# Performance work log

Hardware: AMD Instinct MI355X
Metric: run time of the kernel (lower is better)

Reference implementation:

```python
import jax, jax.numpy as jnp
import numpy as np

N_X = 3
NE = 2048
Emin = 1.0
Emax = 100.0


def setup_inputs() -> dict:
    key = jax.random.key(0)
    k1, k2, k3, k4 = jax.random.split(key, 4)
    # log-spaced energy grid (MeV); code assumes E_grid[0] == Emin
    E_grid = jnp.logspace(np.log10(Emin), np.log10(Emax), NE, dtype=jnp.float32)
    # rates O(1), kernels small -> diagonally dominant per-step system, stable recursion
    R = 1.0 + jax.random.uniform(k1, (N_X, NE), dtype=jnp.float32)
    K = 1e-3 * jax.random.uniform(k2, (N_X, N_X, NE, NE), dtype=jnp.float32)
    S0 = jax.random.uniform(k3, (N_X,), dtype=jnp.float32)
    SC = jax.random.uniform(k4, (N_X, NE), dtype=jnp.float32)
    T = jnp.float32(0.01)
    return {"E_grid": E_grid, "R": R, "K": K, "S0": S0, "SC": SC, "T": T}


def _solve_cascade(E_grid, R, K, S0, SC, T):
    n_x, ne = R.shape
    dy = jnp.log(E_grid[-1] / Emin) / (ne - 1)

    src_last = S0 / R[:, -1]  # (N_X,) : S0[Xp] / R[Xp, -1]
    # boundary value at highest energy: FX_E0[X] = SC[X,-1]/R[X,-1] + sum_Xp K[X,Xp,-1,-1]*S0[Xp]/(R[Xp,-1]*R[X,-1])
    FX_E0 = SC[:, -1] / R[:, -1] + (K[:, :, -1, -1] @ src_last) / R[:, -1]
    F0 = jnp.zeros((n_x, ne), dtype=E_grid.dtype).at[:, -1].set(FX_E0)

    jidx = jnp.arange(ne)

    def step(F, i):
        Ki = K[:, :, i, :]  # (N_X, N_X, NE) slice at outer grid point i
        # trapezoid weights over j: dy*E[j] for i < j < NE-1, half-weight at j = NE-1, 0 elsewhere
        w = jnp.where((jidx > i) & (jidx < ne - 1), dy * E_grid, jnp.zeros((), E_grid.dtype))
        w = w.at[-1].set(0.5 * dy * E_grid[-1])
        # a[X] = SC[X,i] + sum_Xp,j Ki[X,Xp,j] * w[j] * F[Xp,j] + sum_Xp Ki[X,Xp,-1]*S0[Xp]/R[Xp,-1]
        a = SC[:, i] + jnp.einsum('xpj,pj->x', Ki, w * F) + Ki[:, :, -1] @ src_last
        # B[X,Xp] = -0.5*dy*E[i]*K[X,Xp,i,i] + R[X,i]*delta(X,Xp)
        B = -0.5 * dy * E_grid[i] * Ki[:, :, i] + jnp.diag(R[:, i])
        F = F.at[:, i].set(jnp.linalg.solve(B, a))
        return F, None

    idx = jnp.arange(ne - 2, -1, -1)  # backward sweep i = NE-2 ... 0
    F_grid, _ = jax.lax.scan(step, F0, idx)

    approx_zero = jnp.asarray(1e-200, F_grid.dtype)  # underflows to 0 in fp32, matching clamp intent
    F_grid = jnp.where(F_grid > approx_zero, F_grid, approx_zero)

    # sol: row 0 = E_grid, rows 1..N_X = spectra
    return jnp.concatenate([E_grid[None, :], F_grid], axis=0)


def reference(E_grid, R, K, S0, SC, T):
    return _solve_cascade(E_grid, R, K, S0, SC, T)
```

## Files before the change

### kernel.cpp

```cpp
#include <hip/hip_runtime.h>
#include <cstddef>
#include <cstdint>

#define NE 2048
#define NX 3
#define NROWS (NE - 1)
#define BS 64
#define BR (3 * BS)
#define NBLK 32
#define NPAIR 16
#define NCH 8
#define CHS 8
#define CHQ (CHS * 9 * BS)
#define TTH 512
#define PERTH (CHQ / TTH)


static __device__ __forceinline__ float dy_of(const float* E) {
    return logf(E[NE - 1] / E[0]) / (float)(NE - 1);
}

#define DOT4(a, b) ((a).x * (b).x + (a).y * (b).y + (a).z * (b).z + (a).w * (b).w)
#define FMA4(acc, s, b) { (acc).x += (s) * (b).x; (acc).y += (s) * (b).y; \
                          (acc).z += (s) * (b).z; (acc).w += (s) * (b).w; }

__global__ void k_init(const float* __restrict__ E, const float* __restrict__ R,
                       const float* __restrict__ K, const float* __restrict__ S0,
                       const float* __restrict__ SC,
                       float* __restrict__ out, float* __restrict__ wf,
                       float* __restrict__ acc) {
    int i = blockIdx.x * blockDim.x + threadIdx.x;
    if (i >= NE) return;
    const size_t PL = (size_t)NE * NE;
    float dy = dy_of(E);
    float wlast = 0.5f * dy * E[NE - 1];
    float srcl[NX], Fl[NX];
#pragma unroll
    for (int p = 0; p < NX; ++p) srcl[p] = S0[p] / R[p * NE + NE - 1];
#pragma unroll
    for (int x = 0; x < NX; ++x) {
        float s = SC[x * NE + NE - 1];
#pragma unroll
        for (int p = 0; p < NX; ++p)
            s += K[(size_t)(x * NX + p) * PL + (size_t)(NE - 1) * NE + (NE - 1)] * srcl[p];
        Fl[x] = s / R[x * NE + NE - 1];
    }
    out[i] = E[i];
    if (i == NE - 1) {
#pragma unroll
        for (int x = 0; x < NX; ++x) {
            out[(1 + x) * NE + i] = Fl[x] > 0.f ? Fl[x] : 0.f;
            wf[x * NE + i] = wlast * Fl[x];
            acc[x * NE + i] = 0.f;
        }
        return;
    }
#pragma unroll
    for (int x = 0; x < NX; ++x) {
        float s = SC[x * NE + i];
#pragma unroll
        for (int p = 0; p < NX; ++p)
            s += K[(size_t)(x * NX + p) * PL + (size_t)i * NE + (NE - 1)] *
                 (wlast * Fl[p] + srcl[p]);
        acc[x * NE + i] = s;
    }
}

__global__ __launch_bounds__(TTH) void k_tinv(const float* __restrict__ E,
                                              const float* __restrict__ R,
                                              const float* __restrict__ K,
                                              float* __restrict__ G) {
    __shared__ float4 Xs4[BS][BS + 1];
    __shared__ float Kst[CHS][BS][12];
    __shared__ float Binv[BS][9];
    __shared__ float wloc[BS];
    const size_t PL = (size_t)NE * NE;
    int b = blockIdx.x;
    int g = blockIdx.y;
    int i0 = b * BS;
    int tid = threadIdx.x;
    float dy = dy_of(E);

    if (tid < BS) {
        int j = i0 + tid;
        wloc[tid] = (j < NE - 1) ? dy * E[j] : 0.f;
        int ii = tid, i = i0 + ii;
        float b00, b01, b02, b10, b11, b12, b20, b21, b22;
        if (i < NROWS) {
            float h = -0.5f * dy * E[i];
            size_t d = (size_t)i * NE + i;
            b00 = h * K[0 * PL + d] + R[0 * NE + i];
            b01 = h * K[1 * PL + d];
            b02 = h * K[2 * PL + d];
            b10 = h * K[3 * PL + d];
            b11 = h * K[4 * PL + d] + R[1 * NE + i];
            b12 = h * K[5 * PL + d];
            b20 = h * K[6 * PL + d];
            b21 = h * K[7 * PL + d];
            b22 = h * K[8 * PL + d] + R[2 * NE + i];
        } else {
            b00 = 1.f; b01 = 0.f; b02 = 0.f;
            b10 = 0.f; b11 = 1.f; b12 = 0.f;
            b20 = 0.f; b21 = 0.f; b22 = 1.f;
        }
        float C00 = b11 * b22 - b12 * b21;
        float C01 = -(b10 * b22 - b12 * b20);
        float C02 = b10 * b21 - b11 * b20;
        float C10 = -(b01 * b22 - b02 * b21);
        float C11 = b00 * b22 - b02 * b20;
        float C12 = -(b00 * b21 - b01 * b20);
        float C20 = b01 * b12 - b02 * b11;
        float C21 = -(b00 * b12 - b02 * b10);
        float C22 = b00 * b11 - b01 * b10;
        float inv = 1.f / (b00 * C00 + b01 * C01 + b02 * C02);
        Binv[ii][0] = C00 * inv; Binv[ii][1] = C10 * inv; Binv[ii][2] = C20 * inv;
        Binv[ii][3] = C01 * inv; Binv[ii][4] = C11 * inv; Binv[ii][5] = C21 * inv;
        Binv[ii][6] = C02 * inv; Binv[ii][7] = C12 * inv; Binv[ii][8] = C22 * inv;
    }
    __syncthreads();

    float rg[PERTH];
#pragma unroll
    for (int k = 0; k < PERTH; ++k) {
        int q = tid + k * TTH;
        int s = q / (9 * BS);
        int pair = (q / BS) % 9;
        int jj = q & (BS - 1);
        int row = i0 + (BS - 1) - s;
        rg[k] = K[(size_t)pair * PL + (size_t)row * NE + (i0 + jj)];
    }

    int cloc = tid >> 3, sub = tid & 7;
    int colb = g * BS + cloc;

    for (int c = 0; c < NCH; ++c) {
        if (c > 0) __syncthreads();
#pragma unroll
        for (int k = 0; k < PERTH; ++k) {
            int q = tid + k * TTH;
            int s = q / (9 * BS);
            int pair = (q / BS) % 9;
            int jj = q & (BS - 1);
            Kst[s][jj][4 * (pair / 3) + (pair % 3)] = rg[k] * wloc[jj];
        }
        __syncthreads();
        if (c + 1 < NCH) {
#pragma unroll
            for (int k = 0; k < PERTH; ++k) {
                int q = tid + k * TTH;
                int s = q / (9 * BS);
                int pair = (q / BS) % 9;
                int jj = q & (BS - 1);
                int row = i0 + (BS - 1) - ((c + 1) * CHS + s);
                rg[k] = K[(size_t)pair * PL + (size_t)row * NE + (i0 + jj)];
            }
        }
        for (int s = 0; s < CHS; ++s) {
            int ii = (BS - 1) - (c * CHS + s);
            int i = i0 + ii;
            float v0 = 0.f, v1 = 0.f, v2 = 0.f;
            if (sub == 0) {
                v0 = (colb == 3 * ii + 0) ? 1.f : 0.f;
                v1 = (colb == 3 * ii + 1) ? 1.f : 0.f;
                v2 = (colb == 3 * ii + 2) ? 1.f : 0.f;
            }
            if (i < NROWS) {
                for (int jj = ii + 1 + sub; jj < BS; jj += 8) {
                    const float* kp = &Kst[s][jj][0];
                    float4 k0 = *(const float4*)(kp);
                    float4 k1 = *(const float4*)(kp + 4);
                    float4 k2 = *(const float4*)(kp + 8);
                    float4 xv = Xs4[jj][cloc];
                    v0 += k0.x * xv.x + k0.y * xv.y + k0.z * xv.z;
                    v1 += k1.x * xv.x + k1.y * xv.y + k1.z * xv.z;
                    v2 += k2.x * xv.x + k2.y * xv.y + k2.z * xv.z;
                }
            }
            v0 += __shfl_xor(v0, 1); v0 += __shfl_xor(v0, 2); v0 += __shfl_xor(v0, 4);
            v1 += __shfl_xor(v1, 1); v1 += __shfl_xor(v1, 2); v1 += __shfl_xor(v1, 4);
            v2 += __shfl_xor(v2, 1); v2 += __shfl_xor(v2, 2); v2 += __shfl_xor(v2, 4);
            if (sub == 0) {
                float f0, f1, f2;
                if (i < NROWS) {
                    const float* bv = Binv[ii];
                    f0 = bv[0] * v0 + bv[1] * v1 + bv[2] * v2;
                    f1 = bv[3] * v0 + bv[4] * v1 + bv[5] * v2;
                    f2 = bv[6] * v0 + bv[7] * v1 + bv[8] * v2;
                } else {
                    f0 = v0; f1 = v1; f2 = v2;
                }
                Xs4[ii][cloc] = make_float4(f0, f1, f2, 0.f);
            }
            __builtin_amdgcn_wave_barrier();
        }
    }
    __syncthreads();
    float* Gb = G + (size_t)b * BR * BR;
    for (int t = tid; t < BS * BR; t += TTH) {
        int cl = t % BS;
        int rp = t / BS;
        int x = rp >> 6, ii = rp & 63;
        int cb = g * BS + cl;
        int jjc = cb / 3, pc = cb % 3;
        Gb[(size_t)rp * BR + (pc * 64 + jjc)] = ((const float*)&Xs4[ii][cl])[x];
    }
}

__global__ __launch_bounds__(256) void k_gops1(const float* __restrict__ K,
                                               const float* __restrict__ G,
                                               float* __restrict__ ops1) {
    int s = blockIdx.x, ty_ = blockIdx.y, tz = blockIdx.z;
    int rt = tz / 3, ct = tz % 3;
    int t = ty_ + 1;
    float* O = ops1 + (size_t)(s * 3 + ty_) * BR * BR;
    int tid = threadIdx.x;
    if (s + t > NBLK - 1) {
        for (int q = tid; q < 64 * 64; q += 256)
            O[(size_t)(rt * 64 + q / 64) * BR + ct * 64 + (q % 64)] = 0.f;
        return;
    }
    const size_t PL = (size_t)NE * NE;
    const float* Ga = G + (size_t)s * BR * BR;
    int tgt0 = (s + t) * 64;
    int tx = tid & 15, ty = tid >> 4;
    int row0 = rt * 64 + ty * 4;
    int c0 = tx * 4;
    bool maskLast = (s + t == NBLK - 1) && (tx == 15);
    float4 acc0 = {0, 0, 0, 0}, acc1 = {0, 0, 0, 0};
    float4 acc2 = {0, 0, 0, 0}, acc3 = {0, 0, 0, 0};
    for (int k0 = 0; k0 < BR; k0 += 4) {
        int x = k0 >> 6;
        const float* Bb = K + (size_t)(x * 3 + ct) * PL +
                          (size_t)(s * 64 + (k0 & 63)) * NE + tgt0 + c0;
        float4 b0 = *(const float4*)(Bb);
        float4 b1 = *(const float4*)(Bb + NE);
        float4 b2 = *(const float4*)(Bb + 2 * NE);
        float4 b3 = *(const float4*)(Bb + 3 * NE);
        if (maskLast) { b0.w = 0.f; b1.w = 0.f; b2.w = 0.f; b3.w = 0.f; }
        float4 a0 = *(const float4*)(Ga + (size_t)(row0 + 0) * BR + k0);
        float4 a1 = *(const float4*)(Ga + (size_t)(row0 + 1) * BR + k0);
        float4 a2 = *(const float4*)(Ga + (size_t)(row0 + 2) * BR + k0);
        float4 a3 = *(const float4*)(Ga + (size_t)(row0 + 3) * BR + k0);
        FMA4(acc0, a0.x, b0); FMA4(acc0, a0.y, b1); FMA4(acc0, a0.z, b2); FMA4(acc0, a0.w, b3);
        FMA4(acc1, a1.x, b0); FMA4(acc1, a1.y, b1); FMA4(acc1, a1.z, b2); FMA4(acc1, a1.w, b3);
        FMA4(acc2, a2.x, b0); FMA4(acc2, a2.y, b1); FMA4(acc2, a2.z, b2); FMA4(acc2, a2.w, b3);
        FMA4(acc3, a3.x, b0); FMA4(acc3, a3.y, b1); FMA4(acc3, a3.z, b2); FMA4(acc3, a3.w, b3);
    }
    float* Ob = O + (size_t)row0 * BR + ct * 64 + c0;
    *(float4*)(Ob + 0 * BR) = acc0;
    *(float4*)(Ob + 1 * BR) = acc1;
    *(float4*)(Ob + 2 * BR) = acc2;
    *(float4*)(Ob + 3 * BR) = acc3;
}

__global__ __launch_bounds__(256) void k_gops2(const float* __restrict__ E,
                                               const float* __restrict__ G,
                                               const float* __restrict__ ops1,
                                               float* __restrict__ pr) {
    int m = blockIdx.x, w = blockIdx.y, tz = blockIdx.z;
    int rt = tz / 3, ct = tz % 3;
    int A = 2 * m, C = 2 * m + 1;
    int tid = threadIdx.x;
    float dy = dy_of(E);
    const float* Asrc = ops1 + (size_t)(A * 3 + 0) * BR * BR;
    const float* Bsrc = (w == 0) ? (G + (size_t)C * BR * BR)
                                 : (ops1 + (size_t)(C * 3 + (w - 1)) * BR * BR);
    const float* Dsrc = (w == 0) ? nullptr : (ops1 + (size_t)(A * 3 + w) * BR * BR);
    float* O = pr + (size_t)(m * 3 + w) * BR * BR;
    int tx = tid & 15, ty = tid >> 4;
    int row0 = rt * 64 + ty * 4;
    int c0 = ct * 64 + tx * 4;
    float4 acc0 = {0, 0, 0, 0}, acc1 = {0, 0, 0, 0};
    float4 acc2 = {0, 0, 0, 0}, acc3 = {0, 0, 0, 0};
    for (int k0 = 0; k0 < BR; k0 += 4) {
        int e0 = C * 64 + (k0 & 63);
        float w0 = (e0 + 0 < NROWS) ? dy * E[e0 + 0] : 0.f;
        float w1 = (e0 + 1 < NROWS) ? dy * E[e0 + 1] : 0.f;
        float w2 = (e0 + 2 < NROWS) ? dy * E[e0 + 2] : 0.f;
        float w3 = (e0 + 3 < NROWS) ? dy * E[e0 + 3] : 0.f;
        const float* Bb = Bsrc + (size_t)k0 * BR + c0;
        float4 b0 = *(const float4*)(Bb + 0 * BR);
        float4 b1 = *(const float4*)(Bb + 1 * BR);
        float4 b2 = *(const float4*)(Bb + 2 * BR);
        float4 b3 = *(const float4*)(Bb + 3 * BR);
        b0.x *= w0; b0.y *= w0; b0.z *= w0; b0.w *= w0;
        b1.x *= w1; b1.y *= w1; b1.z *= w1; b1.w *= w1;
        b2.x *= w2; b2.y *= w2; b2.z *= w2; b2.w *= w2;
        b3.x *= w3; b3.y *= w3; b3.z *= w3; b3.w *= w3;
        float4 a0 = *(const float4*)(Asrc + (size_t)(row0 + 0) * BR + k0);
        float4 a1 = *(const float4*)(Asrc + (size_t)(row0 + 1) * BR + k0);
        float4 a2 = *(const float4*)(Asrc + (size_t)(row0 + 2) * BR + k0);
        float4 a3 = *(const float4*)(Asrc + (size_t)(row0 + 3) * BR + k0);
        FMA4(acc0, a0.x, b0); FMA4(acc0, a0.y, b1); FMA4(acc0, a0.z, b2); FMA4(acc0, a0.w, b3);
        FMA4(acc1, a1.x, b0); FMA4(acc1, a1.y, b1); FMA4(acc1, a1.z, b2); FMA4(acc1, a1.w, b3);
        FMA4(acc2, a2.x, b0); FMA4(acc2, a2.y, b1); FMA4(acc2, a2.z, b2); FMA4(acc2, a2.w, b3);
        FMA4(acc3, a3.x, b0); FMA4(acc3, a3.y, b1); FMA4(acc3, a3.z, b2); FMA4(acc3, a3.w, b3);
    }
    float* Ob = O + (size_t)row0 * BR + c0;
    if (Dsrc) {
        const float* Db = Dsrc + (size_t)row0 * BR + c0;
        float4 d0 = *(const float4*)(Db + 0 * BR);
        float4 d1 = *(const float4*)(Db + 1 * BR);
        float4 d2 = *(const float4*)(Db + 2 * BR);
        float4 d3 = *(const float4*)(Db + 3 * BR);
        acc0.x += d0.x; acc0.y += d0.y; acc0.z += d0.z; acc0.w += d0.w;
        acc1.x += d1.x; acc1.y += d1.y; acc1.z += d1.z; acc1.w += d1.w;
        acc2.x += d2.x; acc2.y += d2.y; acc2.z += d2.z; acc2.w += d2.w;
        acc3.x += d3.x; acc3.y += d3.y; acc3.z += d3.z; acc3.w += d3.w;
    }
    *(float4*)(Ob + 0 * BR) = acc0;
    *(float4*)(Ob + 1 * BR) = acc1;
    *(float4*)(Ob + 2 * BR) = acc2;
    *(float4*)(Ob + 3 * BR) = acc3;
}

__global__ __launch_bounds__(512) void k_pair2(const float* __restrict__ E,
                                               const float* __restrict__ K,
                                               const float* __restrict__ G,
                                               const float* __restrict__ ops1,
                                               const float* __restrict__ pr,
                                               float* __restrict__ acc,
                                               float* __restrict__ wf,
                                               float* __restrict__ out,
                                               int m, int hasV) {
    const size_t PL = (size_t)NE * NE;
    int A = 2 * m, C = 2 * m + 1;
    int tid = threadIdx.x;
    int bid = blockIdx.x;
    int lane = tid & 63, wv = tid >> 6;

    if (bid >= 12) {
        int jbase = (2 * m + 2) * BS;
        int row = (bid - 12) * 8 + wv;
        int j1 = jbase + lane, j2 = j1 + BS;
        float w10 = wf[0 * NE + j1], w11 = wf[1 * NE + j1], w12 = wf[2 * NE + j1];
        float w20 = 0.f, w21 = 0.f, w22 = 0.f;
        if (j2 < NROWS) {
            w20 = wf[0 * NE + j2]; w21 = wf[1 * NE + j2]; w22 = wf[2 * NE + j2];
        }
        const float* Kb1 = K + (size_t)row * NE + j1;
        const float* Kb2 = K + (size_t)row * NE + j2;
        float s0 = Kb1[0 * PL] * w10 + Kb1[1 * PL] * w11 + Kb1[2 * PL] * w12
                 + Kb2[0 * PL] * w20 + Kb2[1 * PL] * w21 + Kb2[2 * PL] * w22;
        float s1 = Kb1[3 * PL] * w10 + Kb1[4 * PL] * w11 + Kb1[5 * PL] * w12
                 + Kb2[3 * PL] * w20 + Kb2[4 * PL] * w21 + Kb2[5 * PL] * w22;
        float s2 = Kb1[6 * PL] * w10 + Kb1[7 * PL] * w11 + Kb1[8 * PL] * w12
                 + Kb2[6 * PL] * w20 + Kb2[7 * PL] * w21 + Kb2[8 * PL] * w22;
#pragma unroll
        for (int d = 32; d; d >>= 1) {
            s0 += __shfl_xor(s0, d);
            s1 += __shfl_xor(s1, d);
            s2 += __shfl_xor(s2, d);
        }
        if (lane == 0) {
            atomicAdd(&acc[0 * NE + row], s0);
            atomicAdd(&acc[1 * NE + row], s1);
            atomicAdd(&acc[2 * NE + row], s2);
        }
        return;
    }

    __shared__ float4 vec4[4][BR / 4];
    float dy = dy_of(E);
    if (tid < BR) {
        int sp = tid >> 6, e = tid & 63;
        ((float*)vec4[0])[tid] = __hip_atomic_load(&acc[sp * NE + C * BS + e],
                                     __ATOMIC_RELAXED, __HIP_MEMORY_SCOPE_AGENT);
        ((float*)vec4[1])[tid] = __hip_atomic_load(&acc[sp * NE + A * BS + e],
                                     __ATOMIC_RELAXED, __HIP_MEMORY_SCOPE_AGENT);
        ((float*)vec4[2])[tid] = hasV ? wf[sp * NE + (2 * m + 2) * BS + e] : 0.f;
        ((float*)vec4[3])[tid] = hasV ? wf[sp * NE + (2 * m + 3) * BS + e] : 0.f;
    }
    __syncthreads();

    int rloc = tid >> 4, sub = tid & 15;
    bool isC = (bid < 6);
    int rbase = (isC ? bid : bid - 6) * 32;
    int row = rbase + rloc;
    int blk = isC ? C : A;

    const float4* m0 = (const float4*)(G + ((size_t)blk * BR + row) * BR) + sub * 3;
    const float4 *m1, *m2, *m3 = nullptr;
    const float4 *x0, *x1, *x2, *x3 = nullptr;
    if (isC) {
        m1 = (const float4*)(ops1 + ((size_t)(C * 3 + 0) * BR + row) * BR) + sub * 3;
        m2 = (const float4*)(ops1 + ((size_t)(C * 3 + 1) * BR + row) * BR) + sub * 3;
        x0 = vec4[0] + sub * 3; x1 = vec4[2] + sub * 3; x2 = vec4[3] + sub * 3;
    } else {
        m1 = (const float4*)(pr + ((size_t)(m * 3 + 0) * BR + row) * BR) + sub * 3;
        m2 = (const float4*)(pr + ((size_t)(m * 3 + 1) * BR + row) * BR) + sub * 3;
        m3 = (const float4*)(pr + ((size_t)(m * 3 + 2) * BR + row) * BR) + sub * 3;
        x0 = vec4[1] + sub * 3; x1 = vec4[0] + sub * 3;
        x2 = vec4[2] + sub * 3; x3 = vec4[3] + sub * 3;
    }
    float s = 0.f;
#pragma unroll
    for (int q = 0; q < 3; ++q) s += DOT4(m0[q], x0[q]);
    if (hasV || !isC) {
#pragma unroll
        for (int q = 0; q < 3; ++q) s += DOT4(m1[q], x1[q]);
    }
    if (hasV) {
#pragma unroll
        for (int q = 0; q < 3; ++q) s += DOT4(m2[q], x2[q]);
        if (!isC) {
#pragma unroll
            for (int q = 0; q < 3; ++q) s += DOT4(m3[q], x3[q]);
        }
    }
    s += __shfl_xor(s, 1); s += __shfl_xor(s, 2);
    s += __shfl_xor(s, 4); s += __shfl_xor(s, 8);
    if (sub == 0) {
        int x = row >> 6, ii = row & 63;
        int i = blk * BS + ii;
        if (i < NROWS) {
            out[(1 + x) * NE + i] = s > 0.f ? s : 0.f;
            wf[x * NE + i] = dy * E[i] * s;
        }
    }
}

extern "C" void kernel_launch(void* const* d_in, const int* in_sizes, int n_in,
                              void* d_out, int out_size, void* d_ws, size_t ws_size,
                              hipStream_t stream) {
    const float* E = (const float*)d_in[0];
    const float* R = (const float*)d_in[1];
    const float* K = (const float*)d_in[2];
    const float* S0 = (const float*)d_in[3];
    const float* SC = (const float*)d_in[4];
    float* out = (float*)d_out;
    float* wf = (float*)d_ws;
    float* acc = wf + NX * NE;
    float* G = acc + NX * NE;
    float* ops1 = G + (size_t)NBLK * BR * BR;
    float* pr = ops1 + (size_t)NBLK * 3 * BR * BR;

    k_init<<<(NE + 255) / 256, 256, 0, stream>>>(E, R, K, S0, SC, out, wf, acc);
    k_tinv<<<dim3(NBLK, 3), TTH, 0, stream>>>(E, R, K, G);
    k_gops1<<<dim3(NBLK, 3, 9), 256, 0, stream>>>(K, G, ops1);
    k_gops2<<<dim3(NPAIR, 3, 9), 256, 0, stream>>>(E, G, ops1, pr);

    for (int m = NPAIR - 1; m >= 0; --m) {
        int nFar = (m < NPAIR - 1) ? m * 16 : 0;
        int hasV = (m < NPAIR - 1) ? 1 : 0;
        k_pair2<<<12 + nFar, 512, 0, stream>>>(E, K, G, ops1, pr, acc, wf, out,
                                               m, hasV);
    }
}
```

Baseline: 243.9 us.

## Build 64-block triangular inverses by recursive merging of 16-row blocks

The serial 64-step back-substitution that builds each diagonal block's inverse in k_tinv is replaced by a hierarchy. 128 blocks each invert a 16-row sub-block, and two merge kernels then combine them into 32-row and 64-row inverses. Each merge uses the block-triangular formula, where the off-diagonal block is -Linv*K*Binv computed as small dense matmuls. This shortens the sequential dependency chain and spreads the work over more workgroups. The cost is two extra launches, extra workspace traffic, and dependence on the workspace being large enough for the new buffers.

```diff
diff --git a/kernel.cpp b/kernel.cpp
--- a/kernel.cpp
+++ b/kernel.cpp
@@ -9,11 +9,6 @@
 #define BR (3 * BS)
 #define NBLK 32
 #define NPAIR 16
-#define NCH 8
-#define CHS 8
-#define CHQ (CHS * 9 * BS)
-#define TTH 512
-#define PERTH (CHQ / TTH)
 
 
 static __device__ __forceinline__ float dy_of(const float* E) {
@@ -66,25 +61,24 @@
     }
 }
 
-__global__ __launch_bounds__(TTH) void k_tinv(const float* __restrict__ E,
-                                              const float* __restrict__ R,
-                                              const float* __restrict__ K,
-                                              float* __restrict__ G) {
-    __shared__ float4 Xs4[BS][BS + 1];
-    __shared__ float Kst[CHS][BS][12];
-    __shared__ float Binv[BS][9];
-    __shared__ float wloc[BS];
+__global__ __launch_bounds__(256) void k_tinv16(const float* __restrict__ E,
+                                                const float* __restrict__ R,
+                                                const float* __restrict__ K,
+                                                float* __restrict__ Gs16) {
+    __shared__ float4 Xs4[16][49];
+    __shared__ float Kst[16][16][12];
+    __shared__ float Binv[16][9];
+    __shared__ float wloc[16];
     const size_t PL = (size_t)NE * NE;
-    int b = blockIdx.x;
-    int g = blockIdx.y;
-    int i0 = b * BS;
+    int sb = blockIdx.x;
+    int i0 = sb * 16;
     int tid = threadIdx.x;
     float dy = dy_of(E);
 
-    if (tid < BS) {
+    if (tid < 16) {
         int j = i0 + tid;
         wloc[tid] = (j < NE - 1) ? dy * E[j] : 0.f;
-        int ii = tid, i = i0 + ii;
+        int i = i0 + tid, ii = tid;
         float b00, b01, b02, b10, b11, b12, b20, b21, b22;
         if (i < NROWS) {
             float h = -0.5f * dy * E[i];
@@ -118,55 +112,28 @@
         Binv[ii][6] = C02 * inv; Binv[ii][7] = C12 * inv; Binv[ii][8] = C22 * inv;
     }
     __syncthreads();
-
-    float rg[PERTH];
-#pragma unroll
-    for (int k = 0; k < PERTH; ++k) {
-        int q = tid + k * TTH;
-        int s = q / (9 * BS);
-        int pair = (q / BS) % 9;
-        int jj = q & (BS - 1);
-        int row = i0 + (BS - 1) - s;
-        rg[k] = K[(size_t)pair * PL + (size_t)row * NE + (i0 + jj)];
-    }
-
-    int cloc = tid >> 3, sub = tid & 7;
-    int colb = g * BS + cloc;
-
-    for (int c = 0; c < NCH; ++c) {
-        if (c > 0) __syncthreads();
-#pragma unroll
-        for (int k = 0; k < PERTH; ++k) {
-            int q = tid + k * TTH;
-            int s = q / (9 * BS);
-            int pair = (q / BS) % 9;
-            int jj = q & (BS - 1);
-            Kst[s][jj][4 * (pair / 3) + (pair % 3)] = rg[k] * wloc[jj];
-        }
-        __syncthreads();
-        if (c + 1 < NCH) {
-#pragma unroll
-            for (int k = 0; k < PERTH; ++k) {
-                int q = tid + k * TTH;
-                int s = q / (9 * BS);
-                int pair = (q / BS) % 9;
-                int jj = q & (BS - 1);
-                int row = i0 + (BS - 1) - ((c + 1) * CHS + s);
-                rg[k] = K[(size_t)pair * PL + (size_t)row * NE + (i0 + jj)];
-            }
-        }
-        for (int s = 0; s < CHS; ++s) {
-            int ii = (BS - 1) - (c * CHS + s);
+    for (int q = tid; q < 16 * 16 * 9; q += 256) {
+        int jj = q & 15;
+        int ii = (q >> 4) & 15;
+        int pair = q >> 8;
+        Kst[ii][jj][4 * (pair / 3) + (pair % 3)] =
+            K[(size_t)pair * PL + (size_t)(i0 + ii) * NE + (i0 + jj)] * wloc[jj];
+    }
+    __syncthreads();
+
+    int cloc = tid >> 2, sub = tid & 3;
+    if (cloc < 48) {
+        for (int ii = 15; ii >= 0; --ii) {
             int i = i0 + ii;
             float v0 = 0.f, v1 = 0.f, v2 = 0.f;
             if (sub == 0) {
-                v0 = (colb == 3 * ii + 0) ? 1.f : 0.f;
-                v1 = (colb == 3 * ii + 1) ? 1.f : 0.f;
-                v2 = (colb == 3 * ii + 2) ? 1.f : 0.f;
+                v0 = (cloc == 0 * 16 + ii) ? 1.f : 0.f;
+                v1 = (cloc == 1 * 16 + ii) ? 1.f : 0.f;
+                v2 = (cloc == 2 * 16 + ii) ? 1.f : 0.f;
             }
             if (i < NROWS) {
-                for (int jj = ii + 1 + sub; jj < BS; jj += 8) {
-                    const float* kp = &Kst[s][jj][0];
+                for (int jj = ii + 1 + sub; jj < 16; jj += 4) {
+                    const float* kp = &Kst[ii][jj][0];
                     float4 k0 = *(const float4*)(kp);
                     float4 k1 = *(const float4*)(kp + 4);
                     float4 k2 = *(const float4*)(kp + 8);
@@ -176,9 +143,9 @@
                     v2 += k2.x * xv.x + k2.y * xv.y + k2.z * xv.z;
                 }
             }
-            v0 += __shfl_xor(v0, 1); v0 += __shfl_xor(v0, 2); v0 += __shfl_xor(v0, 4);
-            v1 += __shfl_xor(v1, 1); v1 += __shfl_xor(v1, 2); v1 += __shfl_xor(v1, 4);
-            v2 += __shfl_xor(v2, 1); v2 += __shfl_xor(v2, 2); v2 += __shfl_xor(v2, 4);
+            v0 += __shfl_xor(v0, 1); v0 += __shfl_xor(v0, 2);
+            v1 += __shfl_xor(v1, 1); v1 += __shfl_xor(v1, 2);
+            v2 += __shfl_xor(v2, 1); v2 += __shfl_xor(v2, 2);
             if (sub == 0) {
                 float f0, f1, f2;
                 if (i < NROWS) {
@@ -195,15 +162,144 @@
         }
     }
     __syncthreads();
-    float* Gb = G + (size_t)b * BR * BR;
-    for (int t = tid; t < BS * BR; t += TTH) {
-        int cl = t % BS;
-        int rp = t / BS;
-        int x = rp >> 6, ii = rp & 63;
-        int cb = g * BS + cl;
-        int jjc = cb / 3, pc = cb % 3;
-        Gb[(size_t)rp * BR + (pc * 64 + jjc)] = ((const float*)&Xs4[ii][cl])[x];
-    }
+    float* Gb = Gs16 + (size_t)sb * 48 * 48;
+    for (int t = tid; t < 48 * 48; t += 256) {
+        int rp = t / 48, c = t % 48;
+        int x = rp >> 4, ii = rp & 15;
+        Gb[t] = ((const float*)&Xs4[ii][c])[x];
+    }
+}
+
+__global__ __launch_bounds__(256) void k_merge48(const float* __restrict__ E,
+                                                 const float* __restrict__ K,
+                                                 const float* __restrict__ Gs16,
+                                                 float* __restrict__ G32) {
+    __shared__ float Ls[48][49], Bs[48][49], Ks[48][49], Ms[48][49];
+    const size_t PL = (size_t)NE * NE;
+    int q = blockIdx.x;
+    int i0 = q * 32;
+    int tid = threadIdx.x;
+    float dy = dy_of(E);
+    const float* GL = Gs16 + (size_t)(2 * q) * 2304;
+    const float* GH = Gs16 + (size_t)(2 * q + 1) * 2304;
+    for (int t = tid; t < 2304; t += 256) {
+        int r = t / 48, c = t % 48;
+        Ls[r][c] = GL[t];
+        Bs[r][c] = GH[t];
+        int x = r >> 4, ii = r & 15, p = c >> 4, jj = c & 15;
+        int j = i0 + 16 + jj;
+        float w = (j < NE - 1) ? dy * E[j] : 0.f;
+        Ks[r][c] = w * K[(size_t)(x * 3 + p) * PL + (size_t)(i0 + ii) * NE + j];
+    }
+    __syncthreads();
+    int tx = tid & 15, ty = tid >> 4;
+    float m[3][3] = {};
+    for (int k = 0; k < 48; ++k) {
+        float a0 = Ks[ty * 3 + 0][k], a1 = Ks[ty * 3 + 1][k], a2 = Ks[ty * 3 + 2][k];
+        float b0 = Bs[k][tx * 3 + 0], b1 = Bs[k][tx * 3 + 1], b2 = Bs[k][tx * 3 + 2];
+        m[0][0] += a0 * b0; m[0][1] += a0 * b1; m[0][2] += a0 * b2;
+        m[1][0] += a1 * b0; m[1][1] += a1 * b1; m[1][2] += a1 * b2;
+        m[2][0] += a2 * b0; m[2][1] += a2 * b1; m[2][2] += a2 * b2;
+    }
+#pragma unroll
+    for (int i = 0; i < 3; ++i)
+#pragma unroll
+        for (int j = 0; j < 3; ++j) Ms[ty * 3 + i][tx * 3 + j] = m[i][j];
+    __syncthreads();
+    float cc[3][3] = {};
+    for (int k = 0; k < 48; ++k) {
+        float a0 = Ls[ty * 3 + 0][k], a1 = Ls[ty * 3 + 1][k], a2 = Ls[ty * 3 + 2][k];
+        float b0 = Ms[k][tx * 3 + 0], b1 = Ms[k][tx * 3 + 1], b2 = Ms[k][tx * 3 + 2];
+        cc[0][0] += a0 * b0; cc[0][1] += a0 * b1; cc[0][2] += a0 * b2;
+        cc[1][0] += a1 * b0; cc[1][1] += a1 * b1; cc[1][2] += a1 * b2;
+        cc[2][0] += a2 * b0; cc[2][1] += a2 * b1; cc[2][2] += a2 * b2;
+    }
+    float* O = G32 + (size_t)q * 96 * 96;
+    for (int t = tid; t < 2304; t += 256) {
+        int r = t / 48, c = t % 48;
+        int x = r >> 4, ii = r & 15, p = c >> 4, jj = c & 15;
+        O[(size_t)(x * 32 + ii) * 96 + (p * 32 + jj)] = Ls[r][c];
+        O[(size_t)(x * 32 + 16 + ii) * 96 + (p * 32 + 16 + jj)] = Bs[r][c];
+        O[(size_t)(x * 32 + 16 + ii) * 96 + (p * 32 + jj)] = 0.f;
+    }
+#pragma unroll
+    for (int i = 0; i < 3; ++i)
+#pragma unroll
+        for (int j = 0; j < 3; ++j) {
+            int r = ty * 3 + i, c = tx * 3 + j;
+            int x = r >> 4, ii = r & 15, p = c >> 4, jj = c & 15;
+            O[(size_t)(x * 32 + ii) * 96 + (p * 32 + 16 + jj)] = cc[i][j];
+        }
+}
+
+__global__ __launch_bounds__(256) void k_merge96(const float* __restrict__ E,
+                                                 const float* __restrict__ K,
+                                                 const float* __restrict__ G32,
+                                                 float* __restrict__ G) {
+    __shared__ float Bs[96][97], Kws[96][97], Ms[96][97];
+    const size_t PL = (size_t)NE * NE;
+    int b = blockIdx.x;
+    int i0 = b * 64;
+    int tid = threadIdx.x;
+    float dy = dy_of(E);
+    const float* GL = G32 + (size_t)(2 * b) * 9216;
+    const float* GH = G32 + (size_t)(2 * b + 1) * 9216;
+    for (int t = tid; t < 9216; t += 256) {
+        int r = t / 96, k = t % 96;
+        Bs[r][k] = GH[t];
+        int x = r / 32, ii = r % 32, p = k / 32, jj = k % 32;
+        int j = i0 + 32 + jj;
+        float w = (j < NE - 1) ? dy * E[j] : 0.f;
+        Kws[r][k] = w * K[(size_t)(x * 3 + p) * PL + (size_t)(i0 + ii) * NE + j];
+    }
+    __syncthreads();
+    int tx = tid & 15, ty = tid >> 4;
+    float m[6][6] = {};
+    for (int k = 0; k < 96; ++k) {
+        float a[6], bb[6];
+#pragma unroll
+        for (int i = 0; i < 6; ++i) a[i] = Kws[ty * 6 + i][k];
+#pragma unroll
+        for (int j = 0; j < 6; ++j) bb[j] = Bs[k][tx * 6 + j];
+#pragma unroll
+        for (int i = 0; i < 6; ++i)
+#pragma unroll
+            for (int j = 0; j < 6; ++j) m[i][j] += a[i] * bb[j];
+    }
+    __syncthreads();
+#pragma unroll
+    for (int i = 0; i < 6; ++i)
+#pragma unroll
+        for (int j = 0; j < 6; ++j) Ms[ty * 6 + i][tx * 6 + j] = m[i][j];
+    __syncthreads();
+    float cc[6][6] = {};
+    for (int k = 0; k < 96; ++k) {
+        float a[6], bb[6];
+#pragma unroll
+        for (int i = 0; i < 6; ++i) a[i] = GL[(size_t)(ty * 6 + i) * 96 + k];
+#pragma unroll
+        for (int j = 0; j < 6; ++j) bb[j] = Ms[k][tx * 6 + j];
+#pragma unroll
+        for (int i = 0; i < 6; ++i)
+#pragma unroll
+            for (int j = 0; j < 6; ++j) cc[i][j] += a[i] * bb[j];
+    }
+    float* O = G + (size_t)b * BR * BR;
+    for (int t = tid; t < 9216; t += 256) {
+        int r = t / 96, c = t % 96;
+        int x = r / 32, er = r % 32, p = c / 32, ec = c % 32;
+        O[(size_t)(x * 64 + er) * BR + (p * 64 + ec)] = GL[t];
+        O[(size_t)(x * 64 + 32 + er) * BR + (p * 64 + 32 + ec)] = Bs[r][c];
+        O[(size_t)(x * 64 + 32 + er) * BR + (p * 64 + ec)] = 0.f;
+    }
+#pragma unroll
+    for (int i = 0; i < 6; ++i)
+#pragma unroll
+        for (int j = 0; j < 6; ++j) {
+            int r = ty * 6 + i, c = tx * 6 + j;
+            int x = r / 32, er = r % 32, p = c / 32, ec = c % 32;
+            O[(size_t)(x * 64 + er) * BR + (p * 64 + 32 + ec)] = cc[i][j];
+        }
 }
 
 __global__ __launch_bounds__(256) void k_gops1(const float* __restrict__ K,
@@ -434,9 +530,13 @@
     float* G = acc + NX * NE;
     float* ops1 = G + (size_t)NBLK * BR * BR;
     float* pr = ops1 + (size_t)NBLK * 3 * BR * BR;
+    float* Gs16 = pr + (size_t)NPAIR * 3 * BR * BR;
+    float* G32 = Gs16 + (size_t)128 * 48 * 48;
 
     k_init<<<(NE + 255) / 256, 256, 0, stream>>>(E, R, K, S0, SC, out, wf, acc);
-    k_tinv<<<dim3(NBLK, 3), TTH, 0, stream>>>(E, R, K, G);
+    k_tinv16<<<128, 256, 0, stream>>>(E, R, K, Gs16);
+    k_merge48<<<64, 256, 0, stream>>>(E, K, Gs16, G32);
+    k_merge96<<<32, 256, 0, stream>>>(E, K, G32, G);
     k_gops1<<<dim3(NBLK, 3, 9), 256, 0, stream>>>(K, G, ops1);
     k_gops2<<<dim3(NPAIR, 3, 9), 256, 0, stream>>>(E, G, ops1, pr);
 
```

Measured after the change: 248.9 us. 1.02x slower.
